# Optimization experiments

Hardware: AMD Instinct MI355X
Metric: run time of the kernel (lower is better)

Reference implementation:

```python
import math
import jax, jax.numpy as jnp
import numpy as np

B, S, E = 8, 4096, 512


def setup_inputs() -> dict:
    key = jax.random.key(0)
    ks = jax.random.split(key, 8)
    w = 0.02
    return {
        "state1": jax.random.normal(ks[0], (B, S, E), jnp.float32),
        "state2": jax.random.normal(ks[1], (B, S, E), jnp.float32),
        "Wq": jax.random.normal(ks[2], (E, E), jnp.float32) * w,
        "bq": jax.random.normal(ks[3], (E,), jnp.float32) * w,
        "Wk": jax.random.normal(ks[4], (E, E), jnp.float32) * w,
        "bk": jax.random.normal(ks[5], (E,), jnp.float32) * w,
        "Wv": jax.random.normal(ks[6], (E, E), jnp.float32) * w,
        "bv": jax.random.normal(ks[7], (E,), jnp.float32) * w,
    }


def reference(state1, state2, Wq, bq, Wk, bk, Wv, bv):
    b, s, e = state1.shape
    num_blocks = max(1, int(math.ceil(s ** (2.0 / 3.0))))  # 256 for S=4096
    block_size = int(math.ceil(s / num_blocks))            # 16; exact tiling
    scale = math.sqrt(e)

    def proj(x, W, bias):  # torch Linear: x @ W.T + b
        return x @ W.T + bias

    # fold blocks into a batch dimension: [B, nb, bs, E]
    x1 = state1.reshape(b, num_blocks, block_size, e)
    x2 = state2.reshape(b, num_blocks, block_size, e)

    q1, k1, v1 = proj(x1, Wq, bq), proj(x1, Wk, bk), proj(x1, Wv, bv)
    q2, k2, v2 = proj(x2, Wq, bq), proj(x2, Wk, bk), proj(x2, Wv, bv)

    # block-diagonal bidirectional cross attention (dropout = eval/no-op)
    attn12 = jax.nn.softmax(jnp.einsum('bnqe,bnke->bnqk', q1, k2) / scale, axis=-1)
    out1 = jnp.einsum('bnqk,bnke->bnqe', attn12, v2).reshape(b, s, e)

    attn21 = jax.nn.softmax(jnp.einsum('bnqe,bnke->bnqk', q2, k1) / scale, axis=-1)
    out2 = jnp.einsum('bnqk,bnke->bnqe', attn21, v1).reshape(b, s, e)

    return out1, out2
```

## Files before the change

kernel.cpp:

```cpp
#include <hip/hip_runtime.h>
#include <hip/hip_bf16.h>

typedef __attribute__((ext_vector_type(4))) float f32x4;
typedef __attribute__((ext_vector_type(8))) short short8;
typedef __attribute__((ext_vector_type(4))) short short4v;

#define EDIM 512
#define WELEMS 262144

static __device__ __forceinline__ short f2bf(float f) {
  union { float f; unsigned u; } v; v.f = f;
  unsigned r = v.u + 0x7fffu + ((v.u >> 16) & 1u);
  return (short)(r >> 16);
}
static __device__ __forceinline__ float bf2f(short s) {
  union { float f; unsigned u; } v; v.u = ((unsigned)(unsigned short)s) << 16;
  return v.f;
}

static __device__ __forceinline__ void gload_lds16(const short* g, short* l) {
  __builtin_amdgcn_global_load_lds(
      (const __attribute__((address_space(1))) unsigned int*)g,
      (__attribute__((address_space(3))) unsigned int*)(unsigned int)(unsigned long long)l,
      16, 0, 0);
}

__global__ __launch_bounds__(256) void prep_convert(
    const float* __restrict__ s1, const float* __restrict__ s2,
    const float* __restrict__ Wq, const float* __restrict__ bq,
    const float* __restrict__ Wk, const float* __restrict__ Wv,
    short* __restrict__ Wvb, float* __restrict__ tvec, short* __restrict__ Hb,
    short* __restrict__ o1, short* __restrict__ o2, int prep_blocks) {
  __shared__ float sh[2][64][33];
  const int b = blockIdx.x;
  const int tid = threadIdx.x;
  if (b < prep_blocks) {
    if (b < 256) {
      int i = (b * 256 + tid) * 4;
      f32x4 v = *(const f32x4*)(Wv + i);
      short4v vs;
#pragma unroll
      for (int j = 0; j < 4; ++j) vs[j] = f2bf(v[j]);
      *(short4v*)(Wvb + i) = vs;
    } else if (b < 264) {
      float* red = &sh[0][0][0];
      const int fl = tid & 63;
      const int part = tid >> 6;
      const int f = (b - 256) * 64 + fl;
      float s = 0.f;
      const int n0 = part * 128;
#pragma unroll 8
      for (int n = n0; n < n0 + 128; ++n) s += Wk[(size_t)n * EDIM + f] * bq[n];
      red[part * 64 + fl] = s;
      __syncthreads();
      if (part == 0)
        tvec[f] = ((red[fl] + red[64 + fl]) + (red[128 + fl] + red[192 + fl]));
    } else {
      const int hb = b - 264;
      const int bf = (hb >> 4) * 32;
      const int be = (hb & 15) * 32;
      const int fh = (tid & 15) * 2;
      const int eh = (tid >> 4) * 2;
      float a00 = 0, a01 = 0, a10 = 0, a11 = 0;
      for (int nc = 0; nc < 8; ++nc) {
        __syncthreads();
#pragma unroll
        for (int p = 0; p < 8; ++p) {
          const int idx = p * 256 + tid;
          const int n = idx >> 5, f = idx & 31;
          sh[0][n][f] = Wk[(size_t)(nc * 64 + n) * EDIM + bf + f];
          sh[1][n][f] = Wq[(size_t)(nc * 64 + n) * EDIM + be + f];
        }
        __syncthreads();
#pragma unroll 4
        for (int n = 0; n < 64; ++n) {
          const float k0 = sh[0][n][fh], k1 = sh[0][n][fh + 1];
          const float q0 = sh[1][n][eh], q1 = sh[1][n][eh + 1];
          a00 += k0 * q0; a01 += k0 * q1; a10 += k1 * q0; a11 += k1 * q1;
        }
      }
      Hb[(size_t)(bf + fh) * EDIM + be + eh] = f2bf(a00);
      Hb[(size_t)(bf + fh) * EDIM + be + eh + 1] = f2bf(a01);
      Hb[(size_t)(bf + fh + 1) * EDIM + be + eh] = f2bf(a10);
      Hb[(size_t)(bf + fh + 1) * EDIM + be + eh + 1] = f2bf(a11);
    }
  } else {
    const int cb = b - prep_blocks;
    const int wv = tid >> 6, lane = tid & 63;
    const size_t r = (size_t)cb * 4 + wv;
    const int off = lane * 8;
#pragma unroll
    for (int st = 0; st < 2; ++st) {
      const float* src = st ? s2 : s1;
      f32x4 a0 = *(const f32x4*)(src + r * EDIM + off);
      f32x4 a1 = *(const f32x4*)(src + r * EDIM + off + 4);
      short8 rb;
#pragma unroll
      for (int j = 0; j < 4; ++j) { rb[j] = f2bf(a0[j]); rb[j + 4] = f2bf(a1[j]); }
      *(short8*)((st ? o2 : o1) + r * EDIM + off) = rb;
    }
  }
}

__global__ __launch_bounds__(256, 3) void proj_t(
    const short* __restrict__ S1b, const short* __restrict__ S2b,
    const short* __restrict__ Hb,
    short* __restrict__ TV, size_t McE, int mblocks) {
  __shared__ short Al[128 * 64];
  __shared__ short Bl[128 * 64];

  int mb, zn;
  {
    const int L = blockIdx.x;
    if ((mblocks & 7) == 0) {
      const int mpx = mblocks >> 3;
      const int xcd = L & 7;
      const int slot = L >> 3;
      mb = xcd * mpx + slot / 8;
      zn = slot % 8;
    } else { mb = L / 8; zn = L % 8; }
  }
  const int z = zn >> 2;
  const int nb = zn & 3;

  const short* __restrict__ X = z ? S2b : S1b;
  short* __restrict__ O = TV + (size_t)z * McE;

  const int m0 = mb * 128;
  const int n0 = nb * 128;
  const int tid = threadIdx.x;
  const int lane = tid & 63;
  const int wv = tid >> 6;
  const int wr = wv >> 1, wc = wv & 1;
  const int col = lane & 15;
  const int kg = lane >> 4;

  f32x4 acc[4][4] = {};

  for (int ks = 0; ks < EDIM / 64; ++ks) {
    const int k0 = ks * 64;
    __syncthreads();
#pragma unroll
    for (int j = 0; j < 4; ++j) {
      const int g = (j * 4 + wv) * 64 + lane;
      const int row = g >> 3;
      const int sc = (g & 7) ^ (row & 7);
      gload_lds16(X + (size_t)(m0 + row) * EDIM + k0 + sc * 8, Al + (j * 4 + wv) * 512);
      gload_lds16(Hb + (size_t)(n0 + row) * EDIM + k0 + sc * 8, Bl + (j * 4 + wv) * 512);
    }
    __syncthreads();
#pragma unroll
    for (int kk = 0; kk < 2; ++kk) {
      short8 af[4], bf8[4];
#pragma unroll
      for (int i = 0; i < 4; ++i) {
        const int ra = wr * 64 + i * 16 + col;
        const int rb = wc * 64 + i * 16 + col;
        af[i]  = *(const short8*)(Al + ra * 64 + ((((kk << 2) + kg) ^ (ra & 7)) << 3));
        bf8[i] = *(const short8*)(Bl + rb * 64 + ((((kk << 2) + kg) ^ (rb & 7)) << 3));
      }
#pragma unroll
      for (int mi = 0; mi < 4; ++mi)
#pragma unroll
        for (int nj = 0; nj < 4; ++nj)
          acc[mi][nj] = __builtin_amdgcn_mfma_f32_16x16x32_bf16(af[mi], bf8[nj], acc[mi][nj], 0, 0, 0);
    }
  }

#pragma unroll
  for (int mi = 0; mi < 4; ++mi) {
#pragma unroll
    for (int j = 0; j < 4; ++j) {
      const size_t r = m0 + wr * 64 + mi * 16 + kg * 4 + j;
#pragma unroll
      for (int nj = 0; nj < 4; ++nj) {
        const int e = n0 + wc * 64 + nj * 16 + col;
        O[r * EDIM + e] = f2bf(acc[mi][nj][j]);
      }
    }
  }
}

__global__ __launch_bounds__(256) void attn_y(
    const short* __restrict__ TV, const short* __restrict__ S1b, const short* __restrict__ S2b,
    const float* __restrict__ tvec, size_t McE) {
  __shared__ float plds[4][16][16];
  const int dir = blockIdx.y;
  const short* __restrict__ Q = TV + (size_t)dir * McE;
  const short* __restrict__ KV = dir ? S1b : S2b;
  short* __restrict__ Y = (short*)TV + (size_t)(2 + dir) * McE;

  const int lane = threadIdx.x & 63;
  const int wv = threadIdx.x >> 6;
  const size_t r0 = ((size_t)blockIdx.x * 4 + wv) * 16;
  const int col = lane & 15;
  const int kg = lane >> 4;

  const short* Qp = Q + (r0 + col) * EDIM + kg * 8;
  const short* Kp = KV + (r0 + col) * EDIM + kg * 8;
  f32x4 s = {};
  float wp = 0.f;
#pragma unroll
  for (int ks = 0; ks < 16; ++ks) {
    short8 a = *(const short8*)(Qp + ks * 32);
    short8 b = *(const short8*)(Kp + ks * 32);
    const f32x4 t0 = *(const f32x4*)(tvec + ks * 32 + kg * 8);
    const f32x4 t1 = *(const f32x4*)(tvec + ks * 32 + kg * 8 + 4);
#pragma unroll
    for (int i = 0; i < 4; ++i)
      wp += bf2f(b[i]) * t0[i] + bf2f(b[i + 4]) * t1[i];
    s = __builtin_amdgcn_mfma_f32_16x16x32_bf16(a, b, s, 0, 0, 0);
  }
  wp += __shfl_xor(wp, 16);
  wp += __shfl_xor(wp, 32);

  const float scale = 0.04419417382415922f;
  float p[4];
#pragma unroll
  for (int j = 0; j < 4; ++j) p[j] = (s[j] + wp) * scale;
#pragma unroll
  for (int j = 0; j < 4; ++j) {
    float m = p[j];
#pragma unroll
    for (int d = 1; d < 16; d <<= 1) m = fmaxf(m, __shfl_xor(m, d));
    float e = __expf(p[j] - m);
    float ssum = e;
#pragma unroll
    for (int d = 1; d < 16; d <<= 1) ssum += __shfl_xor(ssum, d);
    p[j] = e / ssum;
  }
#pragma unroll
  for (int j = 0; j < 4; ++j) plds[wv][kg * 4 + j][col] = p[j];
  __syncthreads();

  const int e0 = lane * 8;
  short8 v8[16];
#pragma unroll
  for (int k = 0; k < 16; ++k) v8[k] = *(const short8*)(KV + (r0 + k) * EDIM + e0);
#pragma unroll
  for (int q = 0; q < 16; ++q) {
    float acc[8] = {0, 0, 0, 0, 0, 0, 0, 0};
#pragma unroll
    for (int k = 0; k < 16; ++k) {
      const float pv = plds[wv][q][k];
#pragma unroll
      for (int i = 0; i < 8; ++i) acc[i] += pv * bf2f(v8[k][i]);
    }
    short8 y;
#pragma unroll
    for (int i = 0; i < 8; ++i) y[i] = f2bf(acc[i]);
    *(short8*)(Y + (r0 + q) * EDIM + e0) = y;
  }
}

__global__ __launch_bounds__(256, 3) void out_gemm(
    const short* __restrict__ TV, const short* __restrict__ Wvb,
    const float* __restrict__ bv,
    float* __restrict__ out1, float* __restrict__ out2, size_t McE, int mblocks) {
  __shared__ short Al[128 * 64];
  __shared__ short Bl[128 * 64];

  int mb, zn;
  {
    const int L = blockIdx.x;
    if ((mblocks & 7) == 0) {
      const int mpx = mblocks >> 3;
      const int xcd = L & 7;
      const int slot = L >> 3;
      mb = xcd * mpx + slot / 8;
      zn = slot % 8;
    } else { mb = L / 8; zn = L % 8; }
  }
  const int z = zn >> 2;
  const int nb = zn & 3;

  const short* __restrict__ A = TV + (size_t)(2 + z) * McE;
  float* __restrict__ O = z ? out2 : out1;

  const int m0 = mb * 128;
  const int n0 = nb * 128;
  const int tid = threadIdx.x;
  const int lane = tid & 63;
  const int wv = tid >> 6;
  const int wr = wv >> 1, wc = wv & 1;
  const int col = lane & 15;
  const int kg = lane >> 4;

  f32x4 acc[4][4] = {};

  for (int ks = 0; ks < EDIM / 64; ++ks) {
    const int k0 = ks * 64;
    __syncthreads();
#pragma unroll
    for (int j = 0; j < 4; ++j) {
      const int g = (j * 4 + wv) * 64 + lane;
      const int row = g >> 3;
      const int sc = (g & 7) ^ (row & 7);
      gload_lds16(A + (size_t)(m0 + row) * EDIM + k0 + sc * 8, Al + (j * 4 + wv) * 512);
      gload_lds16(Wvb + (size_t)(n0 + row) * EDIM + k0 + sc * 8, Bl + (j * 4 + wv) * 512);
    }
    __syncthreads();
#pragma unroll
    for (int kk = 0; kk < 2; ++kk) {
      short8 af[4], bf8[4];
#pragma unroll
      for (int i = 0; i < 4; ++i) {
        const int ra = wr * 64 + i * 16 + col;
        const int rb = wc * 64 + i * 16 + col;
        af[i]  = *(const short8*)(Al + ra * 64 + ((((kk << 2) + kg) ^ (ra & 7)) << 3));
        bf8[i] = *(const short8*)(Bl + rb * 64 + ((((kk << 2) + kg) ^ (rb & 7)) << 3));
      }
#pragma unroll
      for (int mi = 0; mi < 4; ++mi)
#pragma unroll
        for (int nj = 0; nj < 4; ++nj)
          acc[mi][nj] = __builtin_amdgcn_mfma_f32_16x16x32_bf16(af[mi], bf8[nj], acc[mi][nj], 0, 0, 0);
    }
  }

#pragma unroll
  for (int mi = 0; mi < 4; ++mi) {
#pragma unroll
    for (int j = 0; j < 4; ++j) {
      const size_t r = m0 + wr * 64 + mi * 16 + kg * 4 + j;
#pragma unroll
      for (int nj = 0; nj < 4; ++nj) {
        const int e = n0 + wc * 64 + nj * 16 + col;
        O[r * EDIM + e] = acc[mi][nj][j] + bv[e];
      }
    }
  }
}

extern "C" void kernel_launch(void* const* d_in, const int* in_sizes, int n_in,
                              void* d_out, int out_size, void* d_ws, size_t ws_size,
                              hipStream_t stream) {
  const float* state1 = (const float*)d_in[0];
  const float* state2 = (const float*)d_in[1];
  const float* Wq = (const float*)d_in[2];
  const float* bq = (const float*)d_in[3];
  const float* Wk = (const float*)d_in[4];
  const float* Wv = (const float*)d_in[6];
  const float* bv = (const float*)d_in[7];

  const size_t Mtot = (size_t)8 * 4096;
  float* out1 = (float*)d_out;
  float* out2 = out1 + Mtot * EDIM;

  short* Wvb = (short*)d_ws;
  short* Hb = Wvb + WELEMS;
  float* tvec = (float*)(Hb + WELEMS);
  short* base = (short*)(tvec + EDIM);

  const size_t fixed_bytes = (size_t)(2 * WELEMS) * 2 + EDIM * 4;
  size_t nch = 1;
  while (nch < 256) {
    size_t need = fixed_bytes + (size_t)6 * (Mtot / nch) * EDIM * 2;
    if (need <= ws_size) break;
    nch <<= 1;
  }
  const size_t Mc = Mtot / nch;
  const size_t McE = Mc * EDIM;
  const int mblocks = (int)(Mc / 128);
  short* S1b = base;
  short* S2b = S1b + McE;
  short* TV = S2b + McE;

  for (size_t c = 0; c < nch; ++c) {
    const size_t roff = c * Mc;
    const int pb = (c == 0) ? 520 : 0;
    prep_convert<<<dim3((unsigned)(Mc / 4 + pb)), dim3(256), 0, stream>>>(
        state1 + roff * EDIM, state2 + roff * EDIM, Wq, bq, Wk, Wv,
        Wvb, tvec, Hb, S1b, S2b, pb);
    proj_t<<<dim3((unsigned)(mblocks * 8)), dim3(256), 0, stream>>>(
        S1b, S2b, Hb, TV, McE, mblocks);
    attn_y<<<dim3((unsigned)(Mc / 64), 2), dim3(256), 0, stream>>>(
        TV, S1b, S2b, tvec, McE);
    out_gemm<<<dim3((unsigned)(mblocks * 8)), dim3(256), 0, stream>>>(
        TV, Wvb, bv, out1 + roff * EDIM, out2 + roff * EDIM, McE, mblocks);
  }
}
```

Before: 183.9 us.

## Fuse fp32-to-bf16 input conversion into projection GEMM with register prefetch

Removes the separate conversion pass over state1/state2. The projection GEMM now reads fp32 activations directly, converts them in registers, and writes them to a double-buffered LDS tile. The nb==0 blocks also store the bf16 copy that attn_y needs. The Hb operand is now read straight from global memory instead of staged in LDS, the weight prep is launched once outside the chunk loop, and out_gemm's occupancy hint is raised. The trade-offs: each A tile's fp32 data is read by four N-blocks instead of bf16 once, and unstaged global B loads may hurt MFMA feed.

```diff
diff --git a/kernel.cpp b/kernel.cpp
--- a/kernel.cpp
+++ b/kernel.cpp
@@ -25,89 +25,70 @@
       16, 0, 0);
 }
 
-__global__ __launch_bounds__(256) void prep_convert(
-    const float* __restrict__ s1, const float* __restrict__ s2,
+__global__ __launch_bounds__(256) void prep(
     const float* __restrict__ Wq, const float* __restrict__ bq,
     const float* __restrict__ Wk, const float* __restrict__ Wv,
-    short* __restrict__ Wvb, float* __restrict__ tvec, short* __restrict__ Hb,
-    short* __restrict__ o1, short* __restrict__ o2, int prep_blocks) {
+    short* __restrict__ Wvb, float* __restrict__ tvec, short* __restrict__ Hb) {
   __shared__ float sh[2][64][33];
   const int b = blockIdx.x;
   const int tid = threadIdx.x;
-  if (b < prep_blocks) {
-    if (b < 256) {
-      int i = (b * 256 + tid) * 4;
-      f32x4 v = *(const f32x4*)(Wv + i);
-      short4v vs;
-#pragma unroll
-      for (int j = 0; j < 4; ++j) vs[j] = f2bf(v[j]);
-      *(short4v*)(Wvb + i) = vs;
-    } else if (b < 264) {
-      float* red = &sh[0][0][0];
-      const int fl = tid & 63;
-      const int part = tid >> 6;
-      const int f = (b - 256) * 64 + fl;
-      float s = 0.f;
-      const int n0 = part * 128;
+  if (b < 256) {
+    int i = (b * 256 + tid) * 4;
+    f32x4 v = *(const f32x4*)(Wv + i);
+    short4v vs;
+#pragma unroll
+    for (int j = 0; j < 4; ++j) vs[j] = f2bf(v[j]);
+    *(short4v*)(Wvb + i) = vs;
+  } else if (b < 264) {
+    float* red = &sh[0][0][0];
+    const int fl = tid & 63;
+    const int part = tid >> 6;
+    const int f = (b - 256) * 64 + fl;
+    float s = 0.f;
+    const int n0 = part * 128;
 #pragma unroll 8
-      for (int n = n0; n < n0 + 128; ++n) s += Wk[(size_t)n * EDIM + f] * bq[n];
-      red[part * 64 + fl] = s;
+    for (int n = n0; n < n0 + 128; ++n) s += Wk[(size_t)n * EDIM + f] * bq[n];
+    red[part * 64 + fl] = s;
+    __syncthreads();
+    if (part == 0)
+      tvec[f] = ((red[fl] + red[64 + fl]) + (red[128 + fl] + red[192 + fl]));
+  } else {
+    const int hb = b - 264;
+    const int bf = (hb >> 4) * 32;
+    const int be = (hb & 15) * 32;
+    const int fh = (tid & 15) * 2;
+    const int eh = (tid >> 4) * 2;
+    float a00 = 0, a01 = 0, a10 = 0, a11 = 0;
+    for (int nc = 0; nc < 8; ++nc) {
       __syncthreads();
-      if (part == 0)
-        tvec[f] = ((red[fl] + red[64 + fl]) + (red[128 + fl] + red[192 + fl]));
-    } else {
-      const int hb = b - 264;
-      const int bf = (hb >> 4) * 32;
-      const int be = (hb & 15) * 32;
-      const int fh = (tid & 15) * 2;
-      const int eh = (tid >> 4) * 2;
-      float a00 = 0, a01 = 0, a10 = 0, a11 = 0;
-      for (int nc = 0; nc < 8; ++nc) {
-        __syncthreads();
-#pragma unroll
-        for (int p = 0; p < 8; ++p) {
-          const int idx = p * 256 + tid;
-          const int n = idx >> 5, f = idx & 31;
-          sh[0][n][f] = Wk[(size_t)(nc * 64 + n) * EDIM + bf + f];
-          sh[1][n][f] = Wq[(size_t)(nc * 64 + n) * EDIM + be + f];
-        }
-        __syncthreads();
+#pragma unroll
+      for (int p = 0; p < 8; ++p) {
+        const int idx = p * 256 + tid;
+        const int n = idx >> 5, f = idx & 31;
+        sh[0][n][f] = Wk[(size_t)(nc * 64 + n) * EDIM + bf + f];
+        sh[1][n][f] = Wq[(size_t)(nc * 64 + n) * EDIM + be + f];
+      }
+      __syncthreads();
 #pragma unroll 4
-        for (int n = 0; n < 64; ++n) {
-          const float k0 = sh[0][n][fh], k1 = sh[0][n][fh + 1];
-          const float q0 = sh[1][n][eh], q1 = sh[1][n][eh + 1];
-          a00 += k0 * q0; a01 += k0 * q1; a10 += k1 * q0; a11 += k1 * q1;
-        }
-      }
-      Hb[(size_t)(bf + fh) * EDIM + be + eh] = f2bf(a00);
-      Hb[(size_t)(bf + fh) * EDIM + be + eh + 1] = f2bf(a01);
-      Hb[(size_t)(bf + fh + 1) * EDIM + be + eh] = f2bf(a10);
-      Hb[(size_t)(bf + fh + 1) * EDIM + be + eh + 1] = f2bf(a11);
-    }
-  } else {
-    const int cb = b - prep_blocks;
-    const int wv = tid >> 6, lane = tid & 63;
-    const size_t r = (size_t)cb * 4 + wv;
-    const int off = lane * 8;
-#pragma unroll
-    for (int st = 0; st < 2; ++st) {
-      const float* src = st ? s2 : s1;
-      f32x4 a0 = *(const f32x4*)(src + r * EDIM + off);
-      f32x4 a1 = *(const f32x4*)(src + r * EDIM + off + 4);
-      short8 rb;
-#pragma unroll
-      for (int j = 0; j < 4; ++j) { rb[j] = f2bf(a0[j]); rb[j + 4] = f2bf(a1[j]); }
-      *(short8*)((st ? o2 : o1) + r * EDIM + off) = rb;
-    }
-  }
-}
-
-__global__ __launch_bounds__(256, 3) void proj_t(
-    const short* __restrict__ S1b, const short* __restrict__ S2b,
+      for (int n = 0; n < 64; ++n) {
+        const float k0 = sh[0][n][fh], k1 = sh[0][n][fh + 1];
+        const float q0 = sh[1][n][eh], q1 = sh[1][n][eh + 1];
+        a00 += k0 * q0; a01 += k0 * q1; a10 += k1 * q0; a11 += k1 * q1;
+      }
+    }
+    Hb[(size_t)(bf + fh) * EDIM + be + eh] = f2bf(a00);
+    Hb[(size_t)(bf + fh) * EDIM + be + eh + 1] = f2bf(a01);
+    Hb[(size_t)(bf + fh + 1) * EDIM + be + eh] = f2bf(a10);
+    Hb[(size_t)(bf + fh + 1) * EDIM + be + eh + 1] = f2bf(a11);
+  }
+}
+
+__global__ __launch_bounds__(256, 3) void proj_tc(
+    const float* __restrict__ X1, const float* __restrict__ X2,
     const short* __restrict__ Hb,
+    short* __restrict__ S1b, short* __restrict__ S2b,
     short* __restrict__ TV, size_t McE, int mblocks) {
-  __shared__ short Al[128 * 64];
-  __shared__ short Bl[128 * 64];
+  __shared__ short Al[2][8192];
 
   int mb, zn;
   {
@@ -120,11 +101,12 @@
       zn = slot % 8;
     } else { mb = L / 8; zn = L % 8; }
   }
-  const int z = zn >> 2;
+  const int dir = zn >> 2;
   const int nb = zn & 3;
 
-  const short* __restrict__ X = z ? S2b : S1b;
-  short* __restrict__ O = TV + (size_t)z * McE;
+  const float* __restrict__ X = dir ? X2 : X1;
+  short* __restrict__ Sx = dir ? S2b : S1b;
+  short* __restrict__ O = TV + (size_t)dir * McE;
 
   const int m0 = mb * 128;
   const int n0 = nb * 128;
@@ -135,29 +117,51 @@
   const int col = lane & 15;
   const int kg = lane >> 4;
 
+  const int arow = tid >> 4;
+  const int acol = (tid & 15) * 4;
+  const int g16 = tid & 15;
+  const int chk = g16 >> 1, half = g16 & 1;
+
+  f32x4 an[8];
   f32x4 acc[4][4] = {};
 
-  for (int ks = 0; ks < EDIM / 64; ++ks) {
-    const int k0 = ks * 64;
-    __syncthreads();
-#pragma unroll
-    for (int j = 0; j < 4; ++j) {
-      const int g = (j * 4 + wv) * 64 + lane;
-      const int row = g >> 3;
-      const int sc = (g & 7) ^ (row & 7);
-      gload_lds16(X + (size_t)(m0 + row) * EDIM + k0 + sc * 8, Al + (j * 4 + wv) * 512);
-      gload_lds16(Hb + (size_t)(n0 + row) * EDIM + k0 + sc * 8, Bl + (j * 4 + wv) * 512);
-    }
-    __syncthreads();
+#define LOADA(K0)                                                              \
+  _Pragma("unroll") for (int p = 0; p < 8; ++p)                                \
+      an[p] = *(const f32x4*)(X + (size_t)(m0 + p * 16 + arow) * EDIM + (K0) + acol);
+
+#define CVTWR(BUF, K0)                                                         \
+  _Pragma("unroll") for (int p = 0; p < 8; ++p) {                              \
+    const int row = p * 16 + arow;                                             \
+    float2 lo = make_float2(an[p][0], an[p][1]);                               \
+    float2 hi = make_float2(an[p][2], an[p][3]);                               \
+    union { __hip_bfloat162 h[2]; short4v s; } u;                              \
+    u.h[0] = __float22bfloat162_rn(lo);                                        \
+    u.h[1] = __float22bfloat162_rn(hi);                                        \
+    *(short4v*)&Al[BUF][row * 64 + ((chk ^ (row & 7)) << 3) + (half << 2)] = u.s; \
+    if (nb == 0)                                                               \
+      *(short4v*)(Sx + (size_t)(m0 + row) * EDIM + (K0) + acol) = u.s;         \
+  }
+
+  LOADA(0)
+  asm volatile("s_waitcnt vmcnt(0)" ::: "memory");
+  CVTWR(0, 0)
+  __syncthreads();
+
+  int curNot = 0;
+#pragma unroll
+  for (int ks = 0; ks < 8; ++ks) {
+    const int cur = ks & 1;
+    const int k0n = (ks + 1) * 64;
+    if (ks < 7) { LOADA(k0n) }
 #pragma unroll
     for (int kk = 0; kk < 2; ++kk) {
       short8 af[4], bf8[4];
 #pragma unroll
       for (int i = 0; i < 4; ++i) {
         const int ra = wr * 64 + i * 16 + col;
-        const int rb = wc * 64 + i * 16 + col;
-        af[i]  = *(const short8*)(Al + ra * 64 + ((((kk << 2) + kg) ^ (ra & 7)) << 3));
-        bf8[i] = *(const short8*)(Bl + rb * 64 + ((((kk << 2) + kg) ^ (rb & 7)) << 3));
+        af[i] = *(const short8*)&Al[cur][ra * 64 + ((((kk << 2) + kg) ^ (ra & 7)) << 3)];
+        const int rb = n0 + wc * 64 + i * 16 + col;
+        bf8[i] = *(const short8*)(Hb + (size_t)rb * EDIM + ks * 64 + ((kk << 2) + kg) * 8);
       }
 #pragma unroll
       for (int mi = 0; mi < 4; ++mi)
@@ -165,7 +169,19 @@
         for (int nj = 0; nj < 4; ++nj)
           acc[mi][nj] = __builtin_amdgcn_mfma_f32_16x16x32_bf16(af[mi], bf8[nj], acc[mi][nj], 0, 0, 0);
     }
-  }
+    if (ks < 7) {
+      asm volatile("s_waitcnt vmcnt(0)" ::: "memory");
+      __builtin_amdgcn_sched_barrier(0);
+      CVTWR(cur ^ 1, k0n)
+      asm volatile("s_waitcnt lgkmcnt(0)" ::: "memory");
+      __builtin_amdgcn_sched_barrier(0);
+      __builtin_amdgcn_s_barrier();
+      __builtin_amdgcn_sched_barrier(0);
+    }
+  }
+#undef LOADA
+#undef CVTWR
+  (void)curNot;
 
 #pragma unroll
   for (int mi = 0; mi < 4; ++mi) {
@@ -253,7 +269,7 @@
   }
 }
 
-__global__ __launch_bounds__(256, 3) void out_gemm(
+__global__ __launch_bounds__(256, 5) void out_gemm(
     const short* __restrict__ TV, const short* __restrict__ Wvb,
     const float* __restrict__ bv,
     float* __restrict__ out1, float* __restrict__ out2, size_t McE, int mblocks) {
@@ -366,14 +382,12 @@
   short* S2b = S1b + McE;
   short* TV = S2b + McE;
 
+  prep<<<dim3(520), dim3(256), 0, stream>>>(Wq, bq, Wk, Wv, Wvb, tvec, Hb);
+
   for (size_t c = 0; c < nch; ++c) {
     const size_t roff = c * Mc;
-    const int pb = (c == 0) ? 520 : 0;
-    prep_convert<<<dim3((unsigned)(Mc / 4 + pb)), dim3(256), 0, stream>>>(
-        state1 + roff * EDIM, state2 + roff * EDIM, Wq, bq, Wk, Wv,
-        Wvb, tvec, Hb, S1b, S2b, pb);
-    proj_t<<<dim3((unsigned)(mblocks * 8)), dim3(256), 0, stream>>>(
-        S1b, S2b, Hb, TV, McE, mblocks);
+    proj_tc<<<dim3((unsigned)(mblocks * 8)), dim3(256), 0, stream>>>(
+        state1 + roff * EDIM, state2 + roff * EDIM, Hb, S1b, S2b, TV, McE, mblocks);
     attn_y<<<dim3((unsigned)(Mc / 64), 2), dim3(256), 0, stream>>>(
         TV, S1b, S2b, tvec, McE);
     out_gemm<<<dim3((unsigned)(mblocks * 8)), dim3(256), 0, stream>>>(
```

New measurement: 327.5 us. 78.1% more time.
